# Kernel optimization log

Measured on AMD Instinct MI355X. Metric: run time of the kernel, lower is better.

The kernel has to match this reference:

```python
import jax, jax.numpy as jnp
import numpy as np

B, I, H = 16384, 512, 512


def setup_inputs() -> dict:
    key = jax.random.key(0)
    ks = jax.random.split(key, 9)
    std = 1.0 / np.sqrt(H)
    u = lambda k, shape: jax.random.uniform(k, shape, jnp.float32, -std, std)
    return {
        "input": jax.random.normal(ks[0], (B, I), jnp.float32),
        "h_prev": jax.random.normal(ks[1], (B, H), jnp.float32),
        "c_prev": jax.random.normal(ks[2], (B, H), jnp.float32),
        "m_prev": jax.random.normal(ks[3], (B, H), jnp.float32),
        "n_prev": jnp.ones((B, H), jnp.float32),
        "Wxh": u(ks[4], (4 * H, I)),
        "bxh": u(ks[5], (4 * H,)),
        "Whh": u(ks[6], (4 * H, H)),
        "bhh": u(ks[7], (4 * H,)),
    }


def reference(input, h_prev, c_prev, m_prev, n_prev, Wxh, bxh, Whh, bhh):
    # gates = xh(input) + hh(h_prev) -> [B, 4H]
    gates = input @ Wxh.T + bxh + h_prev @ Whh.T + bhh
    ig, fg, zg, og = jnp.split(gates, 4, axis=1)
    z_t = jnp.tanh(zg)
    o_t = jax.nn.sigmoid(og)
    # log-space stabilizer: log(exp(fg)) = fg, log(exp(ig)) = ig
    m_t = jnp.maximum(fg + m_prev, ig)
    i_t = jnp.exp(ig - m_t)
    f_t = jnp.exp(fg + m_prev - m_t)
    c_t = f_t * c_prev + i_t * z_t
    n_t = f_t * n_prev + i_t
    h_t = o_t * (c_t / n_t)
    return (h_t, c_t, m_t, n_t)
```

## Files before the change

kernel.cpp:

```cpp
#include <hip/hip_runtime.h>

#define Bsz 16384
#define Isz 512
#define Hsz 512
#define Ksz 1024
#define N4H 2048

#define BM 128
#define BK 64

typedef __bf16 bf16x8 __attribute__((ext_vector_type(8)));
typedef __bf16 bf16x4 __attribute__((ext_vector_type(4)));
typedef float  f32x4  __attribute__((ext_vector_type(4)));

__device__ __forceinline__ void async_copy16(const void* g, void* l) {
    __builtin_amdgcn_global_load_lds(
        (__attribute__((address_space(1))) void*)g,
        (__attribute__((address_space(3))) void*)l,
        16, 0, 0);
}

__global__ void pack_all(const float* __restrict__ x, const float* __restrict__ h,
                         const float* __restrict__ Wxh, const float* __restrict__ Whh,
                         const float* __restrict__ bxh, const float* __restrict__ bhh,
                         __bf16* __restrict__ Aq, __bf16* __restrict__ Bq,
                         float* __restrict__ bias) {
    if (blockIdx.x < 16384) {
        int idx = blockIdx.x * 256 + threadIdx.x;
        int e   = idx << 2;
        int row = e >> 10, col = e & 1023;
        const float4 v = (col < Isz)
            ? *(const float4*)(x + (size_t)row * Isz + col)
            : *(const float4*)(h + (size_t)row * Hsz + (col - Isz));
        bf16x4 o = { (__bf16)v.x, (__bf16)v.y, (__bf16)v.z, (__bf16)v.w };
        *(bf16x4*)(Aq + (size_t)e) = o;
    } else {
        int idx = (blockIdx.x - 16384) * 256 + threadIdx.x;
        int p   = idx >> 8;
        int k   = (idx & 255) << 2;
        int nb  = p >> 7, n = p & 127;
        int wn  = n >> 6, t = (n >> 4) & 3, c = n & 15;
        int orow = t * Hsz + nb * 32 + wn * 16 + c;
        const float4 v = (k < Isz)
            ? *(const float4*)(Wxh + (size_t)orow * Isz + k)
            : *(const float4*)(Whh + (size_t)orow * Hsz + (k - Isz));
        bf16x4 o = { (__bf16)v.x, (__bf16)v.y, (__bf16)v.z, (__bf16)v.w };
        *(bf16x4*)(Bq + (size_t)p * Ksz + k) = o;
        if ((idx & 255) == 0) bias[p] = bxh[orow] + bhh[orow];
    }
}

__global__ __launch_bounds__(256, 4) void slstm_gemm(
    const __bf16* __restrict__ Aq, const __bf16* __restrict__ Bq,
    const float* __restrict__ bias,
    const float* __restrict__ c_prev, const float* __restrict__ m_prev,
    const float* __restrict__ n_prev, float* __restrict__ out) {

    __shared__ __bf16 As[BM * BK];
    __shared__ __bf16 Bs[BM * BK];

    const int tid  = threadIdx.x;
    const int w    = tid >> 6;
    const int lane = tid & 63;
    const int wm   = w & 1;
    const int wn   = w >> 1;
    const int bm   = blockIdx.x;
    const int nb   = blockIdx.y;

    const __bf16* Ag = Aq + (size_t)bm * BM * Ksz;
    const __bf16* Bg = Bq + (size_t)nb * BM * Ksz;

    f32x4 acc[4][4];
    const f32x4 zero = {0.f, 0.f, 0.f, 0.f};
#pragma unroll
    for (int mi = 0; mi < 4; ++mi)
#pragma unroll
        for (int ni = 0; ni < 4; ++ni) acc[mi][ni] = zero;

    const int srow = (lane >> 3);
    const int scol = ((lane & 7) ^ srow) * 8;

    for (int k0 = 0; k0 < Ksz; k0 += BK) {
        __syncthreads();
#pragma unroll
        for (int i = 0; i < 4; ++i) {
            const int chunk = w * 4 + i;
            const int row   = chunk * 8 + srow;
            async_copy16(Ag + (size_t)row * Ksz + k0 + scol, (char*)As + chunk * 1024);
            async_copy16(Bg + (size_t)row * Ksz + k0 + scol, (char*)Bs + chunk * 1024);
        }
        __syncthreads();

#pragma unroll
        for (int kk = 0; kk < 2; ++kk) {
            bf16x8 af[4], bf[4];
#pragma unroll
            for (int mi = 0; mi < 4; ++mi) {
                const int r = wm * 64 + mi * 16 + (lane & 15);
                const int p = (kk * 4 + (lane >> 4)) ^ (r & 7);
                af[mi] = *(const bf16x8*)(As + r * BK + p * 8);
            }
#pragma unroll
            for (int ni = 0; ni < 4; ++ni) {
                const int r = wn * 64 + ni * 16 + (lane & 15);
                const int p = (kk * 4 + (lane >> 4)) ^ (r & 7);
                bf[ni] = *(const bf16x8*)(Bs + r * BK + p * 8);
            }
#pragma unroll
            for (int mi = 0; mi < 4; ++mi)
#pragma unroll
                for (int ni = 0; ni < 4; ++ni)
                    acc[mi][ni] = __builtin_amdgcn_mfma_f32_16x16x32_bf16(
                        af[mi], bf[ni], acc[mi][ni], 0, 0, 0);
        }
    }

    const int hidx = nb * 32 + wn * 16 + (lane & 15);
    const int quad = lane >> 4;

    float bsv[4];
#pragma unroll
    for (int ni = 0; ni < 4; ++ni)
        bsv[ni] = bias[nb * 128 + wn * 64 + ni * 16 + (lane & 15)];

    const size_t BH = (size_t)Bsz * Hsz;

#pragma unroll
    for (int mi = 0; mi < 4; ++mi) {
        const int mbase = bm * 128 + wm * 64 + mi * 16 + quad * 4;
#pragma unroll
        for (int r = 0; r < 4; ++r) {
            const int m = mbase + r;
            const size_t off = (size_t)m * Hsz + hidx;
            const float ig = acc[mi][0][r] + bsv[0];
            const float fg = acc[mi][1][r] + bsv[1];
            const float zg = acc[mi][2][r] + bsv[2];
            const float og = acc[mi][3][r] + bsv[3];
            const float cp = c_prev[off];
            const float mp = m_prev[off];
            const float np = n_prev[off];
            const float zt = tanhf(zg);
            const float ot = 1.f / (1.f + expf(-og));
            const float fm = fg + mp;
            const float mt = fmaxf(fm, ig);
            const float it = expf(ig - mt);
            const float ft = expf(fm - mt);
            const float ct = ft * cp + it * zt;
            const float nt = ft * np + it;
            const float ht = ot * (ct / nt);
            out[off]          = ht;
            out[BH + off]     = ct;
            out[2 * BH + off] = mt;
            out[3 * BH + off] = nt;
        }
    }
}

extern "C" void kernel_launch(void* const* d_in, const int* in_sizes, int n_in,
                              void* d_out, int out_size, void* d_ws, size_t ws_size,
                              hipStream_t stream) {
    const float* input  = (const float*)d_in[0];
    const float* h_prev = (const float*)d_in[1];
    const float* c_prev = (const float*)d_in[2];
    const float* m_prev = (const float*)d_in[3];
    const float* n_prev = (const float*)d_in[4];
    const float* Wxh    = (const float*)d_in[5];
    const float* bxh    = (const float*)d_in[6];
    const float* Whh    = (const float*)d_in[7];
    const float* bhh    = (const float*)d_in[8];
    float* out = (float*)d_out;

    __bf16* Aq   = (__bf16*)d_ws;
    __bf16* Bq   = (__bf16*)((char*)d_ws + (size_t)Bsz * Ksz * 2);
    float*  bias = (float*)((char*)d_ws + (size_t)Bsz * Ksz * 2 + (size_t)N4H * Ksz * 2);

    pack_all<<<16384 + 2048, 256, 0, stream>>>(input, h_prev, Wxh, Whh, bxh, bhh,
                                               Aq, Bq, bias);

    dim3 grid(Bsz / BM, Hsz / 32);
    slstm_gemm<<<grid, 256, 0, stream>>>(Aq, Bq, bias, c_prev, m_prev, n_prev, out);
}
```

Before: 344.5 us.

## Use 256x256 tiles with double-buffered LDS and interleaved async loads and MFMA

Replaces the 128x128 single-buffered GEMM tile with a 256x256 tile computed by 8 waves. Global-to-LDS loads run through a double buffer interleaved with MFMA phases using explicit barriers, waitcnt and setprio, so memory traffic overlaps with compute. Larger tiles reuse each loaded A/B slice across more output and cut global traffic. The cost is higher register pressure (32 accumulators per wave), fewer blocks per CU, and fragile hand-placed synchronization.

Result: no change. 348.0 us (+1.0%).

```diff
diff --git a/kernel.cpp b/kernel.cpp
--- a/kernel.cpp
+++ b/kernel.cpp
@@ -6,7 +6,8 @@
 #define Ksz 1024
 #define N4H 2048
 
-#define BM 128
+#define BM 256
+#define BN 256
 #define BK 64
 
 typedef __bf16 bf16x8 __attribute__((ext_vector_type(8)));
@@ -50,84 +51,161 @@
     }
 }
 
-__global__ __launch_bounds__(256, 4) void slstm_gemm(
+#define CFENCE asm volatile("" ::: "memory")
+#define BARRIER { CFENCE; __builtin_amdgcn_s_barrier(); CFENCE; }
+#define WAITLGKM asm volatile("s_waitcnt lgkmcnt(0)" ::: "memory")
+#define WAITVM4  asm volatile("s_waitcnt vmcnt(4)" ::: "memory")
+
+#define LDS_A(ap, fbase)                                                      \
+    _Pragma("unroll") for (int f = 0; f < 4; ++f)                             \
+    _Pragma("unroll") for (int kk = 0; kk < 2; ++kk)                          \
+        af[f][kk] = *(const bf16x8*)((ap) + (fbase + f) * 1024 + ko[kk]);
+
+#define LDS_B(bp, nbase)                                                      \
+    _Pragma("unroll") for (int n = 0; n < 2; ++n)                             \
+    _Pragma("unroll") for (int kk = 0; kk < 2; ++kk)                          \
+        bf[(nbase) + n][kk] = *(const bf16x8*)((bp) + ((nbase) + n) * 1024 + ko[kk]);
+
+#define MMA(fbase, nbase)                                                     \
+    __builtin_amdgcn_s_setprio(1);                                            \
+    _Pragma("unroll") for (int f = 0; f < 4; ++f)                             \
+    _Pragma("unroll") for (int n = 0; n < 2; ++n)                             \
+    _Pragma("unroll") for (int kk = 0; kk < 2; ++kk)                          \
+        acc[(fbase) + f][(nbase) + n] = __builtin_amdgcn_mfma_f32_16x16x32_bf16( \
+            af[f][kk], bf[(nbase) + n][kk], acc[(fbase) + f][(nbase) + n], 0, 0, 0); \
+    __builtin_amdgcn_s_setprio(0);
+
+#define STAGE(arr, buf, half, src, step)                                      \
+    { async_copy16((src) + (size_t)((half) * 128 + rrow) * Ksz + (step) * 64 + scol, \
+                   (char*)(arr) + (buf) * 32768 + (half) * 16384 + tid * 16); \
+      async_copy16((src) + (size_t)((half) * 128 + 64 + rrow) * Ksz + (step) * 64 + scol, \
+                   (char*)(arr) + (buf) * 32768 + (half) * 16384 + 8192 + tid * 16); }
+
+__global__ __launch_bounds__(512, 2) void slstm_gemm(
     const __bf16* __restrict__ Aq, const __bf16* __restrict__ Bq,
     const float* __restrict__ bias,
     const float* __restrict__ c_prev, const float* __restrict__ m_prev,
     const float* __restrict__ n_prev, float* __restrict__ out) {
 
-    __shared__ __bf16 As[BM * BK];
-    __shared__ __bf16 Bs[BM * BK];
+    __shared__ __bf16 As[2][BM * BK];
+    __shared__ __bf16 Bs[2][BN * BK];
 
     const int tid  = threadIdx.x;
     const int w    = tid >> 6;
     const int lane = tid & 63;
     const int wm   = w & 1;
-    const int wn   = w >> 1;
+    const int wc   = w >> 1;
     const int bm   = blockIdx.x;
-    const int nb   = blockIdx.y;
-
-    const __bf16* Ag = Aq + (size_t)bm * BM * Ksz;
-    const __bf16* Bg = Bq + (size_t)nb * BM * Ksz;
-
-    f32x4 acc[4][4];
+    const int nbb  = blockIdx.y;
+
+    const int lr = lane & 15;
+    const int g0 = lane >> 4;
+    const int px = lr & 7;
+
+    const __bf16* Ag = Aq + (size_t)bm  * BM * Ksz;
+    const __bf16* Bg = Bq + (size_t)nbb * BN * Ksz;
+
+    const int rrow = tid >> 3;
+    const int scol = ((tid & 7) ^ (rrow & 7)) * 8;
+
+    const __bf16* A0p = &As[0][(wm * 128 + lr) * 64];
+    const __bf16* A1p = &As[1][(wm * 128 + lr) * 64];
+    const __bf16* B0p = &Bs[0][(wc * 64 + lr) * 64];
+    const __bf16* B1p = &Bs[1][(wc * 64 + lr) * 64];
+    const int ko[2] = { ((0 * 4 + g0) ^ px) * 8, ((1 * 4 + g0) ^ px) * 8 };
+
+    __bf16* AsB = &As[0][0];
+    __bf16* BsB = &Bs[0][0];
+
+    f32x4 acc[8][4];
     const f32x4 zero = {0.f, 0.f, 0.f, 0.f};
 #pragma unroll
-    for (int mi = 0; mi < 4; ++mi)
+    for (int mi = 0; mi < 8; ++mi)
 #pragma unroll
         for (int ni = 0; ni < 4; ++ni) acc[mi][ni] = zero;
 
-    const int srow = (lane >> 3);
-    const int scol = ((lane & 7) ^ srow) * 8;
-
-    for (int k0 = 0; k0 < Ksz; k0 += BK) {
-        __syncthreads();
-#pragma unroll
-        for (int i = 0; i < 4; ++i) {
-            const int chunk = w * 4 + i;
-            const int row   = chunk * 8 + srow;
-            async_copy16(Ag + (size_t)row * Ksz + k0 + scol, (char*)As + chunk * 1024);
-            async_copy16(Bg + (size_t)row * Ksz + k0 + scol, (char*)Bs + chunk * 1024);
-        }
-        __syncthreads();
-
-#pragma unroll
-        for (int kk = 0; kk < 2; ++kk) {
-            bf16x8 af[4], bf[4];
-#pragma unroll
-            for (int mi = 0; mi < 4; ++mi) {
-                const int r = wm * 64 + mi * 16 + (lane & 15);
-                const int p = (kk * 4 + (lane >> 4)) ^ (r & 7);
-                af[mi] = *(const bf16x8*)(As + r * BK + p * 8);
-            }
-#pragma unroll
-            for (int ni = 0; ni < 4; ++ni) {
-                const int r = wn * 64 + ni * 16 + (lane & 15);
-                const int p = (kk * 4 + (lane >> 4)) ^ (r & 7);
-                bf[ni] = *(const bf16x8*)(Bs + r * BK + p * 8);
-            }
-#pragma unroll
-            for (int mi = 0; mi < 4; ++mi)
-#pragma unroll
-                for (int ni = 0; ni < 4; ++ni)
-                    acc[mi][ni] = __builtin_amdgcn_mfma_f32_16x16x32_bf16(
-                        af[mi], bf[ni], acc[mi][ni], 0, 0, 0);
-        }
+    STAGE(BsB, 0, 0, Bg, 0);
+    STAGE(BsB, 0, 1, Bg, 0);
+    STAGE(AsB, 0, 0, Ag, 0);
+    STAGE(AsB, 0, 1, Ag, 0);
+    STAGE(BsB, 1, 0, Bg, 1);
+    STAGE(BsB, 1, 1, Bg, 1);
+    WAITVM4;
+    BARRIER;
+
+    bf16x8 af[4][2];
+    bf16x8 bf[4][2];
+
+#pragma unroll 1
+    for (int i = 0; i < 8; ++i) {
+        const int ic  = (i < 7) ? i : 6;
+        const int sA1 = 2 * i + 1;
+        const int sB0 = 2 * ic + 2;
+        const int sB1 = 2 * ic + 3;
+
+        LDS_A(A0p, 0);
+        LDS_B(B0p, 0);
+        STAGE(AsB, 1, 0, Ag, sA1);
+        BARRIER; WAITLGKM;
+        MMA(0, 0);
+        BARRIER;
+
+        LDS_B(B0p, 2);
+        STAGE(AsB, 1, 1, Ag, sA1);
+        BARRIER; WAITLGKM;
+        MMA(0, 2);
+        BARRIER;
+
+        LDS_A(A0p, 4);
+        STAGE(BsB, 0, 0, Bg, sB0);
+        BARRIER; WAITLGKM;
+        MMA(4, 2);
+        BARRIER;
+
+        STAGE(BsB, 0, 1, Bg, sB0);
+        BARRIER;
+        MMA(4, 0);
+        WAITVM4;
+        BARRIER;
+
+        LDS_A(A1p, 0);
+        LDS_B(B1p, 0);
+        STAGE(AsB, 0, 0, Ag, sB0);
+        BARRIER; WAITLGKM;
+        MMA(0, 0);
+        BARRIER;
+
+        LDS_B(B1p, 2);
+        STAGE(AsB, 0, 1, Ag, sB0);
+        BARRIER; WAITLGKM;
+        MMA(0, 2);
+        BARRIER;
+
+        LDS_A(A1p, 4);
+        STAGE(BsB, 1, 0, Bg, sB1);
+        BARRIER; WAITLGKM;
+        MMA(4, 2);
+        BARRIER;
+
+        STAGE(BsB, 1, 1, Bg, sB1);
+        BARRIER;
+        MMA(4, 0);
+        WAITVM4;
+        BARRIER;
     }
 
-    const int hidx = nb * 32 + wn * 16 + (lane & 15);
-    const int quad = lane >> 4;
+    const int hidx = (nbb * 2 + (wc >> 1)) * 32 + (wc & 1) * 16 + lr;
 
     float bsv[4];
 #pragma unroll
-    for (int ni = 0; ni < 4; ++ni)
-        bsv[ni] = bias[nb * 128 + wn * 64 + ni * 16 + (lane & 15)];
+    for (int n = 0; n < 4; ++n)
+        bsv[n] = bias[nbb * 256 + wc * 64 + n * 16 + lr];
 
     const size_t BH = (size_t)Bsz * Hsz;
 
 #pragma unroll
-    for (int mi = 0; mi < 4; ++mi) {
-        const int mbase = bm * 128 + wm * 64 + mi * 16 + quad * 4;
+    for (int mi = 0; mi < 8; ++mi) {
+        const int mbase = bm * 256 + wm * 128 + mi * 16 + g0 * 4;
 #pragma unroll
         for (int r = 0; r < 4; ++r) {
             const int m = mbase + r;
@@ -177,6 +255,6 @@
     pack_all<<<16384 + 2048, 256, 0, stream>>>(input, h_prev, Wxh, Whh, bxh, bhh,
                                                Aq, Bq, bias);
 
-    dim3 grid(Bsz / BM, Hsz / 32);
-    slstm_gemm<<<grid, 256, 0, stream>>>(Aq, Bq, bias, c_prev, m_prev, n_prev, out);
-}
+    dim3 grid(Bsz / BM, N4H / BN);
+    slstm_gemm<<<grid, 512, 0, stream>>>(Aq, Bq, bias, c_prev, m_prev, n_prev, out);
+}
```
